# Kernel tuning notes

Measured on AMD Instinct MI355X. Metric: run time of the kernel, lower is better.

Reference implementation:

```python
import jax, jax.numpy as jnp
import numpy as np

N_NODES = 100000
N_EDGES = 1600000
IN_DIM = 128
HEADS = 4
HEAD_DIM = 16  # hidden_dim 64 // 4 heads
HID = HEADS * HEAD_DIM
NEG_SLOPE = 0.2


def setup_inputs() -> dict:
    key = jax.random.key(0)
    ks = jax.random.split(key, 20)
    inp = {
        "x": jax.random.normal(ks[0], (N_NODES, IN_DIM), dtype=jnp.float32),
        "edge_index": jax.random.randint(ks[1], (2, N_EDGES), 0, N_NODES, dtype=jnp.int32),
    }
    dims = [IN_DIM, HID, HID]
    for l in range(3):
        d_in = dims[l]
        sc = 1.0 / np.sqrt(d_in)
        inp[f"w{l}"] = jax.random.normal(ks[2 + 4 * l], (d_in, HID), dtype=jnp.float32) * sc
        inp[f"asrc{l}"] = jax.random.normal(ks[3 + 4 * l], (HEADS, HEAD_DIM), dtype=jnp.float32) * 0.1
        inp[f"adst{l}"] = jax.random.normal(ks[4 + 4 * l], (HEADS, HEAD_DIM), dtype=jnp.float32) * 0.1
        inp[f"b{l}"] = jnp.zeros((HID,), dtype=jnp.float32)
    inp["out_w"] = jax.random.normal(ks[14], (HID, 1), dtype=jnp.float32) * (1.0 / np.sqrt(HID))
    inp["out_b"] = jnp.zeros((1,), dtype=jnp.float32)
    return inp


def _gat_layer(h, src, dst, W, a_src, a_dst, b):
    # h: [N, d_in]; src/dst: [E'] (self-loops already appended)
    n = h.shape[0]
    xh = (h @ W).reshape(n, HEADS, HEAD_DIM)              # [N,H,C]
    al_s = jnp.sum(xh * a_src, axis=-1)                   # [N,H]
    al_d = jnp.sum(xh * a_dst, axis=-1)                   # [N,H]
    e = jax.nn.leaky_relu(al_s[src] + al_d[dst], NEG_SLOPE)  # [E',H]
    # segment-softmax over incoming edges of each destination node
    m = jax.ops.segment_max(e, dst, num_segments=n)       # [N,H]
    p = jnp.exp(e - m[dst])
    z = jax.ops.segment_sum(p, dst, num_segments=n)       # [N,H]
    alpha = p / (z[dst] + 1e-16)                          # [E',H]
    msg = xh[src] * alpha[:, :, None]                     # [E',H,C]
    out = jax.ops.segment_sum(msg, dst, num_segments=n)   # [N,H,C]
    return out.reshape(n, HID) + b


def reference(x, edge_index, w0, asrc0, adst0, b0, w1, asrc1, adst1, b1,
              w2, asrc2, adst2, b2, out_w, out_b):
    n = x.shape[0]
    loops = jnp.arange(n, dtype=edge_index.dtype)
    src = jnp.concatenate([edge_index[0], loops])  # PyG GATConv adds self-loops
    dst = jnp.concatenate([edge_index[1], loops])
    h = x
    params = [(w0, asrc0, adst0, b0), (w1, asrc1, adst1, b1), (w2, asrc2, adst2, b2)]
    for W, a_s, a_d, b in params:
        h = _gat_layer(h, src, dst, W, a_s, a_d, b)
        h = jax.nn.relu(h)
    return (h @ out_w + out_b).squeeze(-1)  # [N]
```

## Files before the change

kernel.cpp:

```cpp
#include <hip/hip_runtime.h>


#define NBMAX 512
#define SCHUNK 4096
#define BCAP 8192

typedef __attribute__((ext_vector_type(8))) short bf16x8;
typedef __attribute__((ext_vector_type(4))) float f32x4;

__device__ inline unsigned short bf16_rtn(float x) {
    union { float f; unsigned u; } a; a.f = x;
    return (unsigned short)((a.u + 0x7FFFu + ((a.u >> 16) & 1u)) >> 16);
}
__device__ inline float bf16_to_f(unsigned short s) {
    union { unsigned u; float f; } b; b.u = ((unsigned)s) << 16;
    return b.f;
}

__global__ __launch_bounds__(256) void k_zero(int* p, int n) {
    int i = blockIdx.x * 256 + threadIdx.x;
    if (i < n) p[i] = 0;
}

__global__ __launch_bounds__(256) void k_bhist(const int* __restrict__ dst, int* __restrict__ bhist, int e) {
    __shared__ unsigned int h[NBMAX];
    int t = threadIdx.x;
    h[t] = 0;
    h[t + 256] = 0;
    __syncthreads();
    for (int i = blockIdx.x * 256 + t; i < e; i += gridDim.x * 256)
        atomicAdd(&h[dst[i] >> 8], 1u);
    __syncthreads();
    if (h[t]) atomicAdd(&bhist[t], (int)h[t]);
    if (h[t + 256]) atomicAdd(&bhist[t + 256], (int)h[t + 256]);
}

__global__ __launch_bounds__(512) void k_bscan(const int* __restrict__ bhist, int* __restrict__ boffs,
                                               int* __restrict__ bfill, int nb, int e) {
    __shared__ int s[NBMAX];
    int t = threadIdx.x;
    int v = (t < nb) ? bhist[t] : 0;
    s[t] = v;
    __syncthreads();
    for (int o = 1; o < 512; o <<= 1) {
        int add = (t >= o) ? s[t - o] : 0;
        __syncthreads();
        s[t] += add;
        __syncthreads();
    }
    boffs[t] = s[t] - v;
    if (t == 511) boffs[512] = s[511];
    bfill[t] = 0;
}

__global__ __launch_bounds__(512) void k_bscatter(const int* __restrict__ src, const int* __restrict__ dst,
                                                  const int* __restrict__ boffs, int* __restrict__ bfill,
                                                  unsigned int* __restrict__ edata, int e) {
    __shared__ unsigned int hist[NBMAX];
    __shared__ unsigned int loc[NBMAX];
    __shared__ int gbase[NBMAX];
    __shared__ unsigned int stmp[NBMAX];
    __shared__ unsigned int sortbuf[SCHUNK];
    __shared__ int posbuf[SCHUNK];
    int t = threadIdx.x;
    int i0 = blockIdx.x * SCHUNK;
    int cnt = min(SCHUNK, e - i0);
    hist[t] = 0;
    __syncthreads();
    for (int j = t; j < cnt; j += 512) atomicAdd(&hist[dst[i0 + j] >> 8], 1u);
    __syncthreads();
    unsigned int v = hist[t];
    stmp[t] = v;
    __syncthreads();
    for (int o = 1; o < 512; o <<= 1) {
        unsigned int add = (t >= o) ? stmp[t - o] : 0;
        __syncthreads();
        stmp[t] += add;
        __syncthreads();
    }
    loc[t] = stmp[t] - v;
    int gb = 0;
    if (v > 0) gb = atomicAdd(&bfill[t], (int)v);
    gbase[t] = boffs[t] + gb - (int)loc[t];
    hist[t] = loc[t];
    __syncthreads();
    for (int j = t; j < cnt; j += 512) {
        int d = dst[i0 + j];
        int s = src[i0 + j];
        int b = d >> 8;
        unsigned int p = atomicAdd(&hist[b], 1u);
        sortbuf[p] = (unsigned int)s | ((unsigned int)(d & 255) << 24);
        posbuf[p] = gbase[b] + (int)p;
    }
    __syncthreads();
    for (int j = t; j < cnt; j += 512) edata[posbuf[j]] = sortbuf[j];
}

__global__ __launch_bounds__(256) void k_bfinal(const unsigned int* __restrict__ edata,
                                                const int* __restrict__ boffs, int* __restrict__ offs,
                                                int* __restrict__ ssrc, int* __restrict__ sdst,
                                                int n, int nb) {
    __shared__ unsigned int hist[256];
    __shared__ unsigned int stmp[256];
    __shared__ unsigned int loc[256];
    __shared__ unsigned int srcbuf[BCAP];
    __shared__ unsigned char dstbuf[BCAP];
    int b = blockIdx.x;
    int t = threadIdx.x;
    int e0 = boffs[b], e1 = boffs[b + 1];
    int cnt = e1 - e0;
    hist[t] = 0;
    __syncthreads();
    for (int j = t; j < cnt; j += 256) atomicAdd(&hist[edata[e0 + j] >> 24], 1u);
    __syncthreads();
    unsigned int v = hist[t];
    stmp[t] = v;
    __syncthreads();
    for (int o = 1; o < 256; o <<= 1) {
        unsigned int add = (t >= o) ? stmp[t - o] : 0;
        __syncthreads();
        stmp[t] += add;
        __syncthreads();
    }
    loc[t] = stmp[t] - v;
    int node = b * 256 + t;
    if (node < n) offs[node] = e0 + (int)loc[t];
    if (b == nb - 1 && t == 0) offs[n] = e1;
    hist[t] = loc[t];
    __syncthreads();
    if (cnt <= BCAP) {
        for (int j = t; j < cnt; j += 256) {
            unsigned int p = edata[e0 + j];
            unsigned int pos = atomicAdd(&hist[p >> 24], 1u);
            srcbuf[pos] = p & 0xFFFFFFu;
            dstbuf[pos] = (unsigned char)(p >> 24);
        }
        __syncthreads();
        for (int j = t; j < cnt; j += 256) {
            ssrc[e0 + j] = (int)srcbuf[j];
            sdst[e0 + j] = b * 256 + (int)dstbuf[j];
        }
    } else {
        for (int j = t; j < cnt; j += 256) {
            unsigned int p = edata[e0 + j];
            unsigned int pos = atomicAdd(&hist[p >> 24], 1u);
            ssrc[e0 + (int)pos] = (int)(p & 0xFFFFFFu);
            sdst[e0 + (int)pos] = b * 256 + (int)(p >> 24);
        }
    }
}

__global__ __launch_bounds__(256) void k_wprep(const float* __restrict__ w0, const float* __restrict__ w1,
                                               const float* __restrict__ w2,
                                               unsigned short* __restrict__ p0h, unsigned short* __restrict__ p0l,
                                               unsigned short* __restrict__ p1h, unsigned short* __restrict__ p1l,
                                               unsigned short* __restrict__ p2h, unsigned short* __restrict__ p2l) {
    int g = blockIdx.x * 256 + threadIdx.x;
    const float* W;
    unsigned short *ph, *pl;
    int idx;
    if (g < 1024) { W = w0; ph = p0h; pl = p0l; idx = g; }
    else if (g < 1536) { W = w1; ph = p1h; pl = p1l; idx = g - 1024; }
    else if (g < 2048) { W = w2; ph = p2h; pl = p2l; idx = g - 1536; }
    else return;
    int ko = idx >> 6, nn = idx & 63;
#pragma unroll
    for (int j = 0; j < 8; ++j) {
        float w = W[(size_t)(ko * 8 + j) * 64 + nn];
        unsigned short hb = bf16_rtn(w);
        ph[(size_t)idx * 8 + j] = hb;
        pl[(size_t)idx * 8 + j] = bf16_rtn(w - bf16_to_f(hb));
    }
}

template <int D_IN>
__global__ __launch_bounds__(256) void k_mgemm(const float* __restrict__ h,
                                               const unsigned short* __restrict__ wph,
                                               const unsigned short* __restrict__ wpl,
                                               const float* __restrict__ asrc, const float* __restrict__ adst,
                                               float* __restrict__ xh, float* __restrict__ als,
                                               float* __restrict__ ald, int n) {
    int t = threadIdx.x;
    int wv = t >> 6, lane = t & 63;
    int quad = lane >> 4, l16 = lane & 15;
    int m0 = blockIdx.x * 64 + wv * 16;
    int node_a = m0 + l16;
    int mm = min(node_a, n - 1);
    const float* hrow = h + (size_t)mm * D_IN + quad * 8;

    f32x4 acc[4];
#pragma unroll
    for (int i = 0; i < 4; ++i) acc[i] = (f32x4){0.f, 0.f, 0.f, 0.f};

    constexpr int KSTEPS = D_IN / 32;
#pragma unroll
    for (int s = 0; s < KSTEPS; ++s) {
        float4 a0 = *(const float4*)(hrow + s * 32);
        float4 a1 = *(const float4*)(hrow + s * 32 + 4);
        float av[8] = {a0.x, a0.y, a0.z, a0.w, a1.x, a1.y, a1.z, a1.w};
        bf16x8 ahi, alo;
#pragma unroll
        for (int j = 0; j < 8; ++j) {
            unsigned short hb = bf16_rtn(av[j]);
            ahi[j] = (short)hb;
            alo[j] = (short)bf16_rtn(av[j] - bf16_to_f(hb));
        }
        const unsigned short* bbase = wph + ((size_t)((s * 4 + quad) * 64 + l16)) * 8;
        const unsigned short* bbasel = wpl + ((size_t)((s * 4 + quad) * 64 + l16)) * 8;
#pragma unroll
        for (int nt = 0; nt < 4; ++nt) {
            bf16x8 bhi = *(const bf16x8*)(bbase + (size_t)nt * 16 * 8);
            bf16x8 blo = *(const bf16x8*)(bbasel + (size_t)nt * 16 * 8);
            acc[nt] = __builtin_amdgcn_mfma_f32_16x16x32_bf16(ahi, bhi, acc[nt], 0, 0, 0);
            acc[nt] = __builtin_amdgcn_mfma_f32_16x16x32_bf16(ahi, blo, acc[nt], 0, 0, 0);
            acc[nt] = __builtin_amdgcn_mfma_f32_16x16x32_bf16(alo, bhi, acc[nt], 0, 0, 0);
        }
    }
#pragma unroll
    for (int nt = 0; nt < 4; ++nt) {
        float as_l = asrc[nt * 16 + l16];
        float ad_l = adst[nt * 16 + l16];
#pragma unroll
        for (int r = 0; r < 4; ++r) {
            int node = m0 + quad * 4 + r;
            float c = acc[nt][r];
            if (node < n) xh[(size_t)node * 64 + nt * 16 + l16] = c;
            float ps = c * as_l, pd = c * ad_l;
            ps += __shfl_xor(ps, 1, 64); pd += __shfl_xor(pd, 1, 64);
            ps += __shfl_xor(ps, 2, 64); pd += __shfl_xor(pd, 2, 64);
            ps += __shfl_xor(ps, 4, 64); pd += __shfl_xor(pd, 4, 64);
            ps += __shfl_xor(ps, 8, 64); pd += __shfl_xor(pd, 8, 64);
            if (l16 == 0 && node < n) {
                als[node * 4 + nt] = ps;
                ald[node * 4 + nt] = pd;
            }
        }
    }
}

__device__ inline float4 lrelu4(float4 v) {
    float4 r;
    r.x = v.x >= 0.f ? v.x : 0.2f * v.x;
    r.y = v.y >= 0.f ? v.y : 0.2f * v.y;
    r.z = v.z >= 0.f ? v.z : 0.2f * v.z;
    r.w = v.w >= 0.f ? v.w : 0.2f * v.w;
    return r;
}

__global__ __launch_bounds__(256) void k_edge(const int* __restrict__ ssrc, const int* __restrict__ sdst,
                                              const float* __restrict__ als, const float* __restrict__ ald,
                                              float* __restrict__ pei, int e) {
    int j = blockIdx.x * 256 + threadIdx.x;
    if (j >= e) return;
    int u = ssrc[j], d = sdst[j];
    float4 alu = *(const float4*)(als + 4 * (size_t)u);
    float4 asd = *(const float4*)(als + 4 * (size_t)d);
    float4 add4 = *(const float4*)(ald + 4 * (size_t)d);
    float4 m4 = lrelu4(make_float4(asd.x + add4.x, asd.y + add4.y, asd.z + add4.z, asd.w + add4.w));
    float4 e4 = lrelu4(make_float4(alu.x + add4.x, alu.y + add4.y, alu.z + add4.z, alu.w + add4.w));
    float4 pe;
    pe.x = __expf(e4.x - m4.x);
    pe.y = __expf(e4.y - m4.y);
    pe.z = __expf(e4.z - m4.z);
    pe.w = __expf(e4.w - m4.w);
    *(float4*)(pei + 4 * (size_t)j) = pe;
}

__global__ __launch_bounds__(256) void k_agg(const float* __restrict__ xh, const float* __restrict__ pei,
                                             const int* __restrict__ offs, const int* __restrict__ ssrc,
                                             const float* __restrict__ bias, float* __restrict__ hout,
                                             const float* __restrict__ outw, const float* __restrict__ outb,
                                             float* __restrict__ fout, int n) {
    __shared__ int s_u[4][64];
    __shared__ float s_pe[4][4][64];
    int wslot = threadIdx.x >> 6;
    int lane = threadIdx.x & 63;
    int v = (blockIdx.x * 256 + threadIdx.x) >> 6;
    if (v >= n) return;
    int head = lane >> 4;
    int* ub = s_u[wslot];
    float* per = s_pe[wslot][head];
    float* pew = &s_pe[wslot][0][lane];

    int start = offs[v], end = offs[v + 1];
    const char* xl = (const char*)(xh + lane);
    float acc = *(const float*)(xl + ((size_t)(unsigned)v << 8));
    float zsum = 0.f;

    for (int s0 = start; s0 < end; s0 += 64) {
        int cnt = min(64, end - s0);
        bool act = lane < cnt;
        int u = v;
        float4 pe = make_float4(0.f, 0.f, 0.f, 0.f);
        if (act) {
            u = ssrc[s0 + lane];
            pe = *(const float4*)(pei + 4 * (size_t)(s0 + lane));
        }
        ub[lane] = u << 8;
        pew[0] = pe.x;
        pew[64] = pe.y;
        pew[128] = pe.z;
        pew[192] = pe.w;
        int ng = (cnt + 3) >> 2;
        int g = 0;
        for (; g + 2 <= ng; g += 2) {
            int4 uu0 = *(const int4*)&ub[g * 4];
            int4 uu1 = *(const int4*)&ub[g * 4 + 4];
            float4 pp0 = *(const float4*)&per[g * 4];
            float4 pp1 = *(const float4*)&per[g * 4 + 4];
            float x0 = *(const float*)(xl + (size_t)(unsigned)uu0.x);
            float x1 = *(const float*)(xl + (size_t)(unsigned)uu0.y);
            float x2 = *(const float*)(xl + (size_t)(unsigned)uu0.z);
            float x3 = *(const float*)(xl + (size_t)(unsigned)uu0.w);
            float x4 = *(const float*)(xl + (size_t)(unsigned)uu1.x);
            float x5 = *(const float*)(xl + (size_t)(unsigned)uu1.y);
            float x6 = *(const float*)(xl + (size_t)(unsigned)uu1.z);
            float x7 = *(const float*)(xl + (size_t)(unsigned)uu1.w);
            zsum += pp0.x + pp0.y + pp0.z + pp0.w;
            zsum += pp1.x + pp1.y + pp1.z + pp1.w;
            acc += pp0.x * x0; acc += pp0.y * x1; acc += pp0.z * x2; acc += pp0.w * x3;
            acc += pp1.x * x4; acc += pp1.y * x5; acc += pp1.z * x6; acc += pp1.w * x7;
        }
        for (; g < ng; ++g) {
            int4 uu = *(const int4*)&ub[g * 4];
            float4 pp = *(const float4*)&per[g * 4];
            float x0 = *(const float*)(xl + (size_t)(unsigned)uu.x);
            float x1 = *(const float*)(xl + (size_t)(unsigned)uu.y);
            float x2 = *(const float*)(xl + (size_t)(unsigned)uu.z);
            float x3 = *(const float*)(xl + (size_t)(unsigned)uu.w);
            zsum += pp.x + pp.y + pp.z + pp.w;
            acc += pp.x * x0; acc += pp.y * x1; acc += pp.z * x2; acc += pp.w * x3;
        }
    }
    float z = 1.f + zsum;
    float o = acc / (z + 1e-16f) + bias[lane];
    o = fmaxf(o, 0.f);
    if (outw) {
        float tsum = o * outw[lane];
#pragma unroll
        for (int d = 32; d; d >>= 1) tsum += __shfl_down(tsum, d, 64);
        if (lane == 0) fout[v] = tsum + outb[0];
    } else {
        hout[((size_t)v << 6) + lane] = o;
    }
}

extern "C" void kernel_launch(void* const* d_in, const int* in_sizes, int n_in,
                              void* d_out, int out_size, void* d_ws, size_t ws_size,
                              hipStream_t stream) {
    const float* x = (const float*)d_in[0];
    const int* ei = (const int*)d_in[1];
    const float* w[3] = {(const float*)d_in[2], (const float*)d_in[6], (const float*)d_in[10]};
    const float* as[3] = {(const float*)d_in[3], (const float*)d_in[7], (const float*)d_in[11]};
    const float* ad[3] = {(const float*)d_in[4], (const float*)d_in[8], (const float*)d_in[12]};
    const float* b[3] = {(const float*)d_in[5], (const float*)d_in[9], (const float*)d_in[13]};
    const float* outw = (const float*)d_in[14];
    const float* outb = (const float*)d_in[15];

    const int N = in_sizes[0] / 128;
    const int E = in_sizes[1] / 2;
    const int* src = ei;
    const int* dst = ei + E;
    const int NB = (N + 255) / 256;

    char* ws = (char*)d_ws;
    auto alloc = [&](size_t bytes) -> void* {
        void* p = (void*)ws;
        ws += (bytes + 255) & ~(size_t)255;
        return p;
    };
    int* bhist = (int*)alloc(NBMAX * 4);
    int* boffs = (int*)alloc((NBMAX + 1) * 4);
    int* bfill = (int*)alloc(NBMAX * 4);
    int* offs = (int*)alloc((size_t)(N + 1) * 4);
    int* ssrc = (int*)alloc((size_t)E * 4);
    int* sdst = (int*)alloc((size_t)E * 4);
    float* pei = (float*)alloc((size_t)E * 4 * 4);
    float* xh = (float*)alloc((size_t)N * 64 * 4);
    float* hbuf = (float*)alloc((size_t)N * 64 * 4);
    float* als = (float*)alloc((size_t)N * 4 * 4);
    float* ald = (float*)alloc((size_t)N * 4 * 4);
    unsigned short* p0h = (unsigned short*)alloc(8192 * 2);
    unsigned short* p0l = (unsigned short*)alloc(8192 * 2);
    unsigned short* p1h = (unsigned short*)alloc(4096 * 2);
    unsigned short* p1l = (unsigned short*)alloc(4096 * 2);
    unsigned short* p2h = (unsigned short*)alloc(4096 * 2);
    unsigned short* p2l = (unsigned short*)alloc(4096 * 2);
    unsigned int* edata = (unsigned int*)xh;

    k_wprep<<<8, 256, 0, stream>>>(w[0], w[1], w[2], p0h, p0l, p1h, p1l, p2h, p2l);
    k_zero<<<(NBMAX + 255) / 256, 256, 0, stream>>>(bhist, NBMAX);
    k_bhist<<<256, 256, 0, stream>>>(dst, bhist, E);
    k_bscan<<<1, 512, 0, stream>>>(bhist, boffs, bfill, NB, E);
    k_bscatter<<<(E + SCHUNK - 1) / SCHUNK, 512, 0, stream>>>(src, dst, boffs, bfill, edata, E);
    k_bfinal<<<NB, 256, 0, stream>>>(edata, boffs, offs, ssrc, sdst, N, NB);

    const int gblocks = (N + 63) / 64;
    const int ablocks = (N + 3) / 4;
    const int eblocks = (E + 255) / 256;

    k_mgemm<128><<<gblocks, 256, 0, stream>>>(x, p0h, p0l, as[0], ad[0], xh, als, ald, N);
    k_edge<<<eblocks, 256, 0, stream>>>(ssrc, sdst, als, ald, pei, E);
    k_agg<<<ablocks, 256, 0, stream>>>(xh, pei, offs, ssrc, b[0], hbuf, nullptr, nullptr, nullptr, N);
    k_mgemm<64><<<gblocks, 256, 0, stream>>>(hbuf, p1h, p1l, as[1], ad[1], xh, als, ald, N);
    k_edge<<<eblocks, 256, 0, stream>>>(ssrc, sdst, als, ald, pei, E);
    k_agg<<<ablocks, 256, 0, stream>>>(xh, pei, offs, ssrc, b[1], hbuf, nullptr, nullptr, nullptr, N);
    k_mgemm<64><<<gblocks, 256, 0, stream>>>(hbuf, p2h, p2l, as[2], ad[2], xh, als, ald, N);
    k_edge<<<eblocks, 256, 0, stream>>>(ssrc, sdst, als, ald, pei, E);
    k_agg<<<ablocks, 256, 0, stream>>>(xh, pei, offs, ssrc, b[2], nullptr, outw, outb, (float*)d_out, N);
}
```

Measured before the change: 447.5 us.

## Fuse edge attention exp computation into aggregation kernel and drop sdst

Removes the separate per-edge kernel that wrote exp scores to a global buffer, and computes the scores inside the aggregation kernel from the per-node attention logits. The softmax shift uses the self-loop logit of the destination node, as before. The sorted destination array is no longer produced, which removes a store stream from the sort. The aggregation inner loop is also unrolled to 16 gathers per iteration to keep more loads in flight. The trade is that the aggregation kernel now does extra gathers of als and exp work per edge, in place of three kernel launches and the global write and read of the score buffer per layer.

After: 442.4 us. Within noise of the previous version (-1.1%).

```diff
diff --git a/kernel.cpp b/kernel.cpp
--- a/kernel.cpp
+++ b/kernel.cpp
@@ -98,13 +98,11 @@
 
 __global__ __launch_bounds__(256) void k_bfinal(const unsigned int* __restrict__ edata,
                                                 const int* __restrict__ boffs, int* __restrict__ offs,
-                                                int* __restrict__ ssrc, int* __restrict__ sdst,
-                                                int n, int nb) {
+                                                int* __restrict__ ssrc, int n, int nb) {
     __shared__ unsigned int hist[256];
     __shared__ unsigned int stmp[256];
     __shared__ unsigned int loc[256];
     __shared__ unsigned int srcbuf[BCAP];
-    __shared__ unsigned char dstbuf[BCAP];
     int b = blockIdx.x;
     int t = threadIdx.x;
     int e0 = boffs[b], e1 = boffs[b + 1];
@@ -133,19 +131,14 @@
             unsigned int p = edata[e0 + j];
             unsigned int pos = atomicAdd(&hist[p >> 24], 1u);
             srcbuf[pos] = p & 0xFFFFFFu;
-            dstbuf[pos] = (unsigned char)(p >> 24);
-        }
-        __syncthreads();
-        for (int j = t; j < cnt; j += 256) {
-            ssrc[e0 + j] = (int)srcbuf[j];
-            sdst[e0 + j] = b * 256 + (int)dstbuf[j];
-        }
+        }
+        __syncthreads();
+        for (int j = t; j < cnt; j += 256) ssrc[e0 + j] = (int)srcbuf[j];
     } else {
         for (int j = t; j < cnt; j += 256) {
             unsigned int p = edata[e0 + j];
             unsigned int pos = atomicAdd(&hist[p >> 24], 1u);
             ssrc[e0 + (int)pos] = (int)(p & 0xFFFFFFu);
-            sdst[e0 + (int)pos] = b * 256 + (int)(p >> 24);
         }
     }
 }
@@ -247,26 +240,8 @@
     return r;
 }
 
-__global__ __launch_bounds__(256) void k_edge(const int* __restrict__ ssrc, const int* __restrict__ sdst,
-                                              const float* __restrict__ als, const float* __restrict__ ald,
-                                              float* __restrict__ pei, int e) {
-    int j = blockIdx.x * 256 + threadIdx.x;
-    if (j >= e) return;
-    int u = ssrc[j], d = sdst[j];
-    float4 alu = *(const float4*)(als + 4 * (size_t)u);
-    float4 asd = *(const float4*)(als + 4 * (size_t)d);
-    float4 add4 = *(const float4*)(ald + 4 * (size_t)d);
-    float4 m4 = lrelu4(make_float4(asd.x + add4.x, asd.y + add4.y, asd.z + add4.z, asd.w + add4.w));
-    float4 e4 = lrelu4(make_float4(alu.x + add4.x, alu.y + add4.y, alu.z + add4.z, alu.w + add4.w));
-    float4 pe;
-    pe.x = __expf(e4.x - m4.x);
-    pe.y = __expf(e4.y - m4.y);
-    pe.z = __expf(e4.z - m4.z);
-    pe.w = __expf(e4.w - m4.w);
-    *(float4*)(pei + 4 * (size_t)j) = pe;
-}
-
-__global__ __launch_bounds__(256) void k_agg(const float* __restrict__ xh, const float* __restrict__ pei,
+__global__ __launch_bounds__(256) void k_agg(const float* __restrict__ xh,
+                                             const float* __restrict__ als, const float* __restrict__ ald,
                                              const int* __restrict__ offs, const int* __restrict__ ssrc,
                                              const float* __restrict__ bias, float* __restrict__ hout,
                                              const float* __restrict__ outw, const float* __restrict__ outb,
@@ -283,18 +258,27 @@
     float* pew = &s_pe[wslot][0][lane];
 
     int start = offs[v], end = offs[v + 1];
+    float4 alsv = *(const float4*)(als + 4 * (size_t)v);
+    float4 aldv = *(const float4*)(ald + 4 * (size_t)v);
+    float4 m4 = lrelu4(make_float4(alsv.x + aldv.x, alsv.y + aldv.y,
+                                   alsv.z + aldv.z, alsv.w + aldv.w));
     const char* xl = (const char*)(xh + lane);
     float acc = *(const float*)(xl + ((size_t)(unsigned)v << 8));
     float zsum = 0.f;
 
     for (int s0 = start; s0 < end; s0 += 64) {
         int cnt = min(64, end - s0);
-        bool act = lane < cnt;
         int u = v;
         float4 pe = make_float4(0.f, 0.f, 0.f, 0.f);
-        if (act) {
+        if (lane < cnt) {
             u = ssrc[s0 + lane];
-            pe = *(const float4*)(pei + 4 * (size_t)(s0 + lane));
+            float4 alu = *(const float4*)(als + 4 * (size_t)u);
+            float4 e4 = lrelu4(make_float4(alu.x + aldv.x, alu.y + aldv.y,
+                                           alu.z + aldv.z, alu.w + aldv.w));
+            pe.x = __expf(e4.x - m4.x);
+            pe.y = __expf(e4.y - m4.y);
+            pe.z = __expf(e4.z - m4.z);
+            pe.w = __expf(e4.w - m4.w);
         }
         ub[lane] = u << 8;
         pew[0] = pe.x;
@@ -303,6 +287,40 @@
         pew[192] = pe.w;
         int ng = (cnt + 3) >> 2;
         int g = 0;
+        for (; g + 4 <= ng; g += 4) {
+            int4 uu0 = *(const int4*)&ub[g * 4];
+            int4 uu1 = *(const int4*)&ub[g * 4 + 4];
+            int4 uu2 = *(const int4*)&ub[g * 4 + 8];
+            int4 uu3 = *(const int4*)&ub[g * 4 + 12];
+            float4 pp0 = *(const float4*)&per[g * 4];
+            float4 pp1 = *(const float4*)&per[g * 4 + 4];
+            float4 pp2 = *(const float4*)&per[g * 4 + 8];
+            float4 pp3 = *(const float4*)&per[g * 4 + 12];
+            float x0 = *(const float*)(xl + (size_t)(unsigned)uu0.x);
+            float x1 = *(const float*)(xl + (size_t)(unsigned)uu0.y);
+            float x2 = *(const float*)(xl + (size_t)(unsigned)uu0.z);
+            float x3 = *(const float*)(xl + (size_t)(unsigned)uu0.w);
+            float x4 = *(const float*)(xl + (size_t)(unsigned)uu1.x);
+            float x5 = *(const float*)(xl + (size_t)(unsigned)uu1.y);
+            float x6 = *(const float*)(xl + (size_t)(unsigned)uu1.z);
+            float x7 = *(const float*)(xl + (size_t)(unsigned)uu1.w);
+            float x8 = *(const float*)(xl + (size_t)(unsigned)uu2.x);
+            float x9 = *(const float*)(xl + (size_t)(unsigned)uu2.y);
+            float xa = *(const float*)(xl + (size_t)(unsigned)uu2.z);
+            float xb = *(const float*)(xl + (size_t)(unsigned)uu2.w);
+            float xc = *(const float*)(xl + (size_t)(unsigned)uu3.x);
+            float xd = *(const float*)(xl + (size_t)(unsigned)uu3.y);
+            float xe = *(const float*)(xl + (size_t)(unsigned)uu3.z);
+            float xf = *(const float*)(xl + (size_t)(unsigned)uu3.w);
+            zsum += pp0.x + pp0.y + pp0.z + pp0.w;
+            zsum += pp1.x + pp1.y + pp1.z + pp1.w;
+            zsum += pp2.x + pp2.y + pp2.z + pp2.w;
+            zsum += pp3.x + pp3.y + pp3.z + pp3.w;
+            acc += pp0.x * x0; acc += pp0.y * x1; acc += pp0.z * x2; acc += pp0.w * x3;
+            acc += pp1.x * x4; acc += pp1.y * x5; acc += pp1.z * x6; acc += pp1.w * x7;
+            acc += pp2.x * x8; acc += pp2.y * x9; acc += pp2.z * xa; acc += pp2.w * xb;
+            acc += pp3.x * xc; acc += pp3.y * xd; acc += pp3.z * xe; acc += pp3.w * xf;
+        }
         for (; g + 2 <= ng; g += 2) {
             int4 uu0 = *(const int4*)&ub[g * 4];
             int4 uu1 = *(const int4*)&ub[g * 4 + 4];
@@ -374,8 +392,6 @@
     int* bfill = (int*)alloc(NBMAX * 4);
     int* offs = (int*)alloc((size_t)(N + 1) * 4);
     int* ssrc = (int*)alloc((size_t)E * 4);
-    int* sdst = (int*)alloc((size_t)E * 4);
-    float* pei = (float*)alloc((size_t)E * 4 * 4);
     float* xh = (float*)alloc((size_t)N * 64 * 4);
     float* hbuf = (float*)alloc((size_t)N * 64 * 4);
     float* als = (float*)alloc((size_t)N * 4 * 4);
@@ -393,19 +409,15 @@
     k_bhist<<<256, 256, 0, stream>>>(dst, bhist, E);
     k_bscan<<<1, 512, 0, stream>>>(bhist, boffs, bfill, NB, E);
     k_bscatter<<<(E + SCHUNK - 1) / SCHUNK, 512, 0, stream>>>(src, dst, boffs, bfill, edata, E);
-    k_bfinal<<<NB, 256, 0, stream>>>(edata, boffs, offs, ssrc, sdst, N, NB);
+    k_bfinal<<<NB, 256, 0, stream>>>(edata, boffs, offs, ssrc, N, NB);
 
     const int gblocks = (N + 63) / 64;
     const int ablocks = (N + 3) / 4;
-    const int eblocks = (E + 255) / 256;
 
     k_mgemm<128><<<gblocks, 256, 0, stream>>>(x, p0h, p0l, as[0], ad[0], xh, als, ald, N);
-    k_edge<<<eblocks, 256, 0, stream>>>(ssrc, sdst, als, ald, pei, E);
-    k_agg<<<ablocks, 256, 0, stream>>>(xh, pei, offs, ssrc, b[0], hbuf, nullptr, nullptr, nullptr, N);
+    k_agg<<<ablocks, 256, 0, stream>>>(xh, als, ald, offs, ssrc, b[0], hbuf, nullptr, nullptr, nullptr, N);
     k_mgemm<64><<<gblocks, 256, 0, stream>>>(hbuf, p1h, p1l, as[1], ad[1], xh, als, ald, N);
-    k_edge<<<eblocks, 256, 0, stream>>>(ssrc, sdst, als, ald, pei, E);
-    k_agg<<<ablocks, 256, 0, stream>>>(xh, pei, offs, ssrc, b[1], hbuf, nullptr, nullptr, nullptr, N);
+    k_agg<<<ablocks, 256, 0, stream>>>(xh, als, ald, offs, ssrc, b[1], hbuf, nullptr, nullptr, nullptr, N);
     k_mgemm<64><<<gblocks, 256, 0, stream>>>(hbuf, p2h, p2l, as[2], ad[2], xh, als, ald, N);
-    k_edge<<<eblocks, 256, 0, stream>>>(ssrc, sdst, als, ald, pei, E);
-    k_agg<<<ablocks, 256, 0, stream>>>(xh, pei, offs, ssrc, b[2], nullptr, outw, outb, (float*)d_out, N);
-}
+    k_agg<<<ablocks, 256, 0, stream>>>(xh, als, ald, offs, ssrc, b[2], nullptr, outw, outb, (float*)d_out, N);
+}
```

## Fuse edge softmax scores into aggregation with padded CSR and four nodes per wave

Applied to the files above, without the earlier changes.

Removes the separate per-edge score kernel and its E×4 float intermediate. Aggregation now recomputes the leaky-relu and exp scores from the node attention logits on the fly. Each node's edge segment is padded to a multiple of four, using a sentinel node with a -1e30 score and zero features, so grouped loads need no masking. The sdst array is dropped, and each wavefront now processes four destination nodes and splits the chunk's edges by node boundaries. This trades extra gathers of als/ald and more complex control flow for fewer launches and less global memory traffic.

New measurement: 434.3 us. 3.0% less time.

```diff
diff --git a/kernel.cpp b/kernel.cpp
--- a/kernel.cpp
+++ b/kernel.cpp
@@ -4,6 +4,7 @@
 #define NBMAX 512
 #define SCHUNK 4096
 #define BCAP 8192
+#define PADSLACK 768
 
 typedef __attribute__((ext_vector_type(8))) short bf16x8;
 typedef __attribute__((ext_vector_type(4))) float f32x4;
@@ -17,9 +18,14 @@
     return b.f;
 }
 
-__global__ __launch_bounds__(256) void k_zero(int* p, int n) {
+__global__ __launch_bounds__(256) void k_init(int* __restrict__ bhist, int nb,
+                                              float* __restrict__ als, float* __restrict__ xh, int n) {
     int i = blockIdx.x * 256 + threadIdx.x;
-    if (i < n) p[i] = 0;
+    if (i < nb) bhist[i] = 0;
+    int j = i - NBMAX;
+    if (j >= 0 && j < 4) als[(size_t)n * 4 + j] = -1e30f;
+    int k = i - NBMAX - 4;
+    if (k >= 0 && k < 64) xh[(size_t)n * 64 + k] = 0.f;
 }
 
 __global__ __launch_bounds__(256) void k_bhist(const int* __restrict__ dst, int* __restrict__ bhist, int e) {
@@ -97,24 +103,27 @@
 }
 
 __global__ __launch_bounds__(256) void k_bfinal(const unsigned int* __restrict__ edata,
-                                                const int* __restrict__ boffs, int* __restrict__ offs,
-                                                int* __restrict__ ssrc, int* __restrict__ sdst,
+                                                const int* __restrict__ boffs, int* __restrict__ poffs,
+                                                int* __restrict__ pend, int* __restrict__ ssrc,
                                                 int n, int nb) {
     __shared__ unsigned int hist[256];
     __shared__ unsigned int stmp[256];
     __shared__ unsigned int loc[256];
+    __shared__ unsigned int cnt_s[256];
     __shared__ unsigned int srcbuf[BCAP];
-    __shared__ unsigned char dstbuf[BCAP];
     int b = blockIdx.x;
     int t = threadIdx.x;
     int e0 = boffs[b], e1 = boffs[b + 1];
     int cnt = e1 - e0;
+    int pb = e0 + b * PADSLACK;
     hist[t] = 0;
     __syncthreads();
     for (int j = t; j < cnt; j += 256) atomicAdd(&hist[edata[e0 + j] >> 24], 1u);
     __syncthreads();
     unsigned int v = hist[t];
-    stmp[t] = v;
+    unsigned int v4 = (v + 3u) & ~3u;
+    cnt_s[t] = v;
+    stmp[t] = v4;
     __syncthreads();
     for (int o = 1; o < 256; o <<= 1) {
         unsigned int add = (t >= o) ? stmp[t - o] : 0;
@@ -122,31 +131,31 @@
         stmp[t] += add;
         __syncthreads();
     }
-    loc[t] = stmp[t] - v;
+    loc[t] = stmp[t] - v4;
+    int ptot = (int)stmp[255];
     int node = b * 256 + t;
-    if (node < n) offs[node] = e0 + (int)loc[t];
-    if (b == nb - 1 && t == 0) offs[n] = e1;
+    if (node < n) {
+        poffs[node] = pb + (int)loc[t];
+        pend[node] = pb + (int)(loc[t] + v4);
+    }
     hist[t] = loc[t];
     __syncthreads();
-    if (cnt <= BCAP) {
+    if (cnt + PADSLACK <= BCAP) {
         for (int j = t; j < cnt; j += 256) {
             unsigned int p = edata[e0 + j];
             unsigned int pos = atomicAdd(&hist[p >> 24], 1u);
             srcbuf[pos] = p & 0xFFFFFFu;
-            dstbuf[pos] = (unsigned char)(p >> 24);
-        }
-        __syncthreads();
-        for (int j = t; j < cnt; j += 256) {
-            ssrc[e0 + j] = (int)srcbuf[j];
-            sdst[e0 + j] = b * 256 + (int)dstbuf[j];
-        }
+        }
+        for (unsigned int k = v; k < v4; ++k) srcbuf[loc[t] + k] = (unsigned int)n;
+        __syncthreads();
+        for (int j = t; j < ptot; j += 256) ssrc[pb + j] = (int)srcbuf[j];
     } else {
         for (int j = t; j < cnt; j += 256) {
             unsigned int p = edata[e0 + j];
             unsigned int pos = atomicAdd(&hist[p >> 24], 1u);
-            ssrc[e0 + (int)pos] = (int)(p & 0xFFFFFFu);
-            sdst[e0 + (int)pos] = b * 256 + (int)(p >> 24);
-        }
+            ssrc[pb + (int)pos] = (int)(p & 0xFFFFFFu);
+        }
+        for (unsigned int k = v; k < v4; ++k) ssrc[pb + (int)(loc[t] + k)] = n;
     }
 }
 
@@ -247,27 +256,59 @@
     return r;
 }
 
-__global__ __launch_bounds__(256) void k_edge(const int* __restrict__ ssrc, const int* __restrict__ sdst,
-                                              const float* __restrict__ als, const float* __restrict__ ald,
-                                              float* __restrict__ pei, int e) {
-    int j = blockIdx.x * 256 + threadIdx.x;
-    if (j >= e) return;
-    int u = ssrc[j], d = sdst[j];
-    float4 alu = *(const float4*)(als + 4 * (size_t)u);
-    float4 asd = *(const float4*)(als + 4 * (size_t)d);
-    float4 add4 = *(const float4*)(ald + 4 * (size_t)d);
-    float4 m4 = lrelu4(make_float4(asd.x + add4.x, asd.y + add4.y, asd.z + add4.z, asd.w + add4.w));
-    float4 e4 = lrelu4(make_float4(alu.x + add4.x, alu.y + add4.y, alu.z + add4.z, alu.w + add4.w));
-    float4 pe;
-    pe.x = __expf(e4.x - m4.x);
-    pe.y = __expf(e4.y - m4.y);
-    pe.z = __expf(e4.z - m4.z);
-    pe.w = __expf(e4.w - m4.w);
-    *(float4*)(pei + 4 * (size_t)j) = pe;
-}
-
-__global__ __launch_bounds__(256) void k_agg(const float* __restrict__ xh, const float* __restrict__ pei,
-                                             const int* __restrict__ offs, const int* __restrict__ ssrc,
+#define ACCUM(LO, HI, ACC, ZS)                                                  \
+    {                                                                           \
+        int g_ = ((LO) - s0) >> 2, gb_ = ((HI) - s0) >> 2;                      \
+        for (; g_ + 4 <= gb_; g_ += 4) {                                        \
+            int4 uu0 = *(const int4*)&ub[g_ * 4];                               \
+            int4 uu1 = *(const int4*)&ub[g_ * 4 + 4];                           \
+            int4 uu2 = *(const int4*)&ub[g_ * 4 + 8];                           \
+            int4 uu3 = *(const int4*)&ub[g_ * 4 + 12];                          \
+            float4 pp0 = *(const float4*)&per[g_ * 4];                          \
+            float4 pp1 = *(const float4*)&per[g_ * 4 + 4];                      \
+            float4 pp2 = *(const float4*)&per[g_ * 4 + 8];                      \
+            float4 pp3 = *(const float4*)&per[g_ * 4 + 12];                     \
+            float x0 = *(const float*)(xl + (size_t)(unsigned)uu0.x);           \
+            float x1 = *(const float*)(xl + (size_t)(unsigned)uu0.y);           \
+            float x2 = *(const float*)(xl + (size_t)(unsigned)uu0.z);           \
+            float x3 = *(const float*)(xl + (size_t)(unsigned)uu0.w);           \
+            float x4 = *(const float*)(xl + (size_t)(unsigned)uu1.x);           \
+            float x5 = *(const float*)(xl + (size_t)(unsigned)uu1.y);           \
+            float x6 = *(const float*)(xl + (size_t)(unsigned)uu1.z);           \
+            float x7 = *(const float*)(xl + (size_t)(unsigned)uu1.w);           \
+            float x8 = *(const float*)(xl + (size_t)(unsigned)uu2.x);           \
+            float x9 = *(const float*)(xl + (size_t)(unsigned)uu2.y);           \
+            float xa = *(const float*)(xl + (size_t)(unsigned)uu2.z);           \
+            float xb = *(const float*)(xl + (size_t)(unsigned)uu2.w);           \
+            float xc = *(const float*)(xl + (size_t)(unsigned)uu3.x);           \
+            float xd = *(const float*)(xl + (size_t)(unsigned)uu3.y);           \
+            float xe = *(const float*)(xl + (size_t)(unsigned)uu3.z);           \
+            float xf = *(const float*)(xl + (size_t)(unsigned)uu3.w);           \
+            ZS += pp0.x + pp0.y + pp0.z + pp0.w;                                \
+            ZS += pp1.x + pp1.y + pp1.z + pp1.w;                                \
+            ZS += pp2.x + pp2.y + pp2.z + pp2.w;                                \
+            ZS += pp3.x + pp3.y + pp3.z + pp3.w;                                \
+            ACC += pp0.x * x0; ACC += pp0.y * x1; ACC += pp0.z * x2; ACC += pp0.w * x3; \
+            ACC += pp1.x * x4; ACC += pp1.y * x5; ACC += pp1.z * x6; ACC += pp1.w * x7; \
+            ACC += pp2.x * x8; ACC += pp2.y * x9; ACC += pp2.z * xa; ACC += pp2.w * xb; \
+            ACC += pp3.x * xc; ACC += pp3.y * xd; ACC += pp3.z * xe; ACC += pp3.w * xf; \
+        }                                                                       \
+        for (; g_ < gb_; ++g_) {                                                \
+            int4 uu = *(const int4*)&ub[g_ * 4];                                \
+            float4 pp = *(const float4*)&per[g_ * 4];                           \
+            float x0 = *(const float*)(xl + (size_t)(unsigned)uu.x);            \
+            float x1 = *(const float*)(xl + (size_t)(unsigned)uu.y);            \
+            float x2 = *(const float*)(xl + (size_t)(unsigned)uu.z);            \
+            float x3 = *(const float*)(xl + (size_t)(unsigned)uu.w);            \
+            ZS += pp.x + pp.y + pp.z + pp.w;                                    \
+            ACC += pp.x * x0; ACC += pp.y * x1; ACC += pp.z * x2; ACC += pp.w * x3; \
+        }                                                                       \
+    }
+
+__global__ __launch_bounds__(256) void k_agg(const float* __restrict__ xh,
+                                             const float* __restrict__ als, const float* __restrict__ ald,
+                                             const int* __restrict__ poffs, const int* __restrict__ pend,
+                                             const int* __restrict__ ssrc,
                                              const float* __restrict__ bias, float* __restrict__ hout,
                                              const float* __restrict__ outw, const float* __restrict__ outb,
                                              float* __restrict__ fout, int n) {
@@ -275,73 +316,93 @@
     __shared__ float s_pe[4][4][64];
     int wslot = threadIdx.x >> 6;
     int lane = threadIdx.x & 63;
-    int v = (blockIdx.x * 256 + threadIdx.x) >> 6;
-    if (v >= n) return;
+    int w = (blockIdx.x * 256 + threadIdx.x) >> 6;
+    int v0 = w << 2;
+    if (v0 >= n) return;
     int head = lane >> 4;
     int* ub = s_u[wslot];
     float* per = s_pe[wslot][head];
     float* pew = &s_pe[wslot][0][lane];
 
-    int start = offs[v], end = offs[v + 1];
+    int vlast = n - 1;
+    int last = min(v0 + 3, vlast);
+    int4 rr = *(const int4*)(poffs + v0);
+    int e3 = pend[last];
+    int r0 = rr.x;
+    int r1 = (v0 + 1 <= last) ? rr.y : e3;
+    int r2 = (v0 + 2 <= last) ? rr.z : e3;
+    int r3 = (v0 + 3 <= last) ? rr.w : e3;
+
     const char* xl = (const char*)(xh + lane);
-    float acc = *(const float*)(xl + ((size_t)(unsigned)v << 8));
-    float zsum = 0.f;
-
-    for (int s0 = start; s0 < end; s0 += 64) {
-        int cnt = min(64, end - s0);
-        bool act = lane < cnt;
-        int u = v;
-        float4 pe = make_float4(0.f, 0.f, 0.f, 0.f);
-        if (act) {
-            u = ssrc[s0 + lane];
-            pe = *(const float4*)(pei + 4 * (size_t)(s0 + lane));
-        }
+    float acc0 = *(const float*)(xl + ((size_t)(unsigned)v0 << 8));
+    float acc1 = *(const float*)(xl + ((size_t)(unsigned)min(v0 + 1, vlast) << 8));
+    float acc2 = *(const float*)(xl + ((size_t)(unsigned)min(v0 + 2, vlast) << 8));
+    float acc3 = *(const float*)(xl + ((size_t)(unsigned)min(v0 + 3, vlast) << 8));
+    float zs0 = 0.f, zs1 = 0.f, zs2 = 0.f, zs3 = 0.f;
+
+    for (int s0 = r0; s0 < e3; s0 += 64) {
+        int cnt = min(64, e3 - s0);
+        int e = s0 + lane;
+        int u = n;
+        if (lane < cnt) u = ssrc[e];
+        int nid = v0 + (e >= r1) + (e >= r2) + (e >= r3);
+        nid = min(nid, vlast);
+        float4 alsd = *(const float4*)(als + 4 * (size_t)nid);
+        float4 aldd = *(const float4*)(ald + 4 * (size_t)nid);
+        float4 m4 = lrelu4(make_float4(alsd.x + aldd.x, alsd.y + aldd.y,
+                                       alsd.z + aldd.z, alsd.w + aldd.w));
+        float4 alu = *(const float4*)(als + 4 * (size_t)u);
+        float4 e4 = lrelu4(make_float4(alu.x + aldd.x, alu.y + aldd.y,
+                                       alu.z + aldd.z, alu.w + aldd.w));
+        float4 pe;
+        pe.x = __expf(e4.x - m4.x);
+        pe.y = __expf(e4.y - m4.y);
+        pe.z = __expf(e4.z - m4.z);
+        pe.w = __expf(e4.w - m4.w);
         ub[lane] = u << 8;
         pew[0] = pe.x;
         pew[64] = pe.y;
         pew[128] = pe.z;
         pew[192] = pe.w;
-        int ng = (cnt + 3) >> 2;
-        int g = 0;
-        for (; g + 2 <= ng; g += 2) {
-            int4 uu0 = *(const int4*)&ub[g * 4];
-            int4 uu1 = *(const int4*)&ub[g * 4 + 4];
-            float4 pp0 = *(const float4*)&per[g * 4];
-            float4 pp1 = *(const float4*)&per[g * 4 + 4];
-            float x0 = *(const float*)(xl + (size_t)(unsigned)uu0.x);
-            float x1 = *(const float*)(xl + (size_t)(unsigned)uu0.y);
-            float x2 = *(const float*)(xl + (size_t)(unsigned)uu0.z);
-            float x3 = *(const float*)(xl + (size_t)(unsigned)uu0.w);
-            float x4 = *(const float*)(xl + (size_t)(unsigned)uu1.x);
-            float x5 = *(const float*)(xl + (size_t)(unsigned)uu1.y);
-            float x6 = *(const float*)(xl + (size_t)(unsigned)uu1.z);
-            float x7 = *(const float*)(xl + (size_t)(unsigned)uu1.w);
-            zsum += pp0.x + pp0.y + pp0.z + pp0.w;
-            zsum += pp1.x + pp1.y + pp1.z + pp1.w;
-            acc += pp0.x * x0; acc += pp0.y * x1; acc += pp0.z * x2; acc += pp0.w * x3;
-            acc += pp1.x * x4; acc += pp1.y * x5; acc += pp1.z * x6; acc += pp1.w * x7;
-        }
-        for (; g < ng; ++g) {
-            int4 uu = *(const int4*)&ub[g * 4];
-            float4 pp = *(const float4*)&per[g * 4];
-            float x0 = *(const float*)(xl + (size_t)(unsigned)uu.x);
-            float x1 = *(const float*)(xl + (size_t)(unsigned)uu.y);
-            float x2 = *(const float*)(xl + (size_t)(unsigned)uu.z);
-            float x3 = *(const float*)(xl + (size_t)(unsigned)uu.w);
-            zsum += pp.x + pp.y + pp.z + pp.w;
-            acc += pp.x * x0; acc += pp.y * x1; acc += pp.z * x2; acc += pp.w * x3;
-        }
-    }
-    float z = 1.f + zsum;
-    float o = acc / (z + 1e-16f) + bias[lane];
-    o = fmaxf(o, 0.f);
+        int lim = s0 + cnt;
+        int hi0 = min(r1, lim);
+        int lo1 = max(r1, s0), hi1 = min(r2, lim);
+        int lo2 = max(r2, s0), hi2 = min(r3, lim);
+        int lo3 = max(r3, s0);
+        ACCUM(s0, hi0, acc0, zs0);
+        ACCUM(lo1, hi1, acc1, zs1);
+        ACCUM(lo2, hi2, acc2, zs2);
+        ACCUM(lo3, lim, acc3, zs3);
+    }
+
+    float bl = bias[lane];
+    float z0 = 1.f + zs0, z1 = 1.f + zs1, z2 = 1.f + zs2, z3 = 1.f + zs3;
+    float o0 = fmaxf(acc0 / (z0 + 1e-16f) + bl, 0.f);
+    float o1 = fmaxf(acc1 / (z1 + 1e-16f) + bl, 0.f);
+    float o2 = fmaxf(acc2 / (z2 + 1e-16f) + bl, 0.f);
+    float o3 = fmaxf(acc3 / (z3 + 1e-16f) + bl, 0.f);
     if (outw) {
-        float tsum = o * outw[lane];
-#pragma unroll
-        for (int d = 32; d; d >>= 1) tsum += __shfl_down(tsum, d, 64);
-        if (lane == 0) fout[v] = tsum + outb[0];
+        float ow = outw[lane];
+        float ob = outb[0];
+        float t0 = o0 * ow, t1 = o1 * ow, t2 = o2 * ow, t3 = o3 * ow;
+#pragma unroll
+        for (int d = 32; d; d >>= 1) {
+            t0 += __shfl_down(t0, d, 64);
+            t1 += __shfl_down(t1, d, 64);
+            t2 += __shfl_down(t2, d, 64);
+            t3 += __shfl_down(t3, d, 64);
+        }
+        if (lane == 0) {
+            fout[v0] = t0 + ob;
+            if (v0 + 1 < n) fout[v0 + 1] = t1 + ob;
+            if (v0 + 2 < n) fout[v0 + 2] = t2 + ob;
+            if (v0 + 3 < n) fout[v0 + 3] = t3 + ob;
+        }
     } else {
-        hout[((size_t)v << 6) + lane] = o;
+        hout[((size_t)v0 << 6) + lane] = o0;
+        if (v0 + 1 < n) hout[((size_t)(v0 + 1) << 6) + lane] = o1;
+        if (v0 + 2 < n) hout[((size_t)(v0 + 2) << 6) + lane] = o2;
+        if (v0 + 3 < n) hout[((size_t)(v0 + 3) << 6) + lane] = o3;
     }
 }
 
@@ -372,13 +433,12 @@
     int* bhist = (int*)alloc(NBMAX * 4);
     int* boffs = (int*)alloc((NBMAX + 1) * 4);
     int* bfill = (int*)alloc(NBMAX * 4);
-    int* offs = (int*)alloc((size_t)(N + 1) * 4);
-    int* ssrc = (int*)alloc((size_t)E * 4);
-    int* sdst = (int*)alloc((size_t)E * 4);
-    float* pei = (float*)alloc((size_t)E * 4 * 4);
-    float* xh = (float*)alloc((size_t)N * 64 * 4);
+    int* poffs = (int*)alloc((size_t)(N + 8) * 4);
+    int* pend = (int*)alloc((size_t)N * 4);
+    int* ssrc = (int*)alloc((size_t)(E + NBMAX * PADSLACK + 256) * 4);
+    float* xh = (float*)alloc((size_t)(N + 1) * 64 * 4);
     float* hbuf = (float*)alloc((size_t)N * 64 * 4);
-    float* als = (float*)alloc((size_t)N * 4 * 4);
+    float* als = (float*)alloc((size_t)(N + 1) * 4 * 4);
     float* ald = (float*)alloc((size_t)N * 4 * 4);
     unsigned short* p0h = (unsigned short*)alloc(8192 * 2);
     unsigned short* p0l = (unsigned short*)alloc(8192 * 2);
@@ -389,23 +449,19 @@
     unsigned int* edata = (unsigned int*)xh;
 
     k_wprep<<<8, 256, 0, stream>>>(w[0], w[1], w[2], p0h, p0l, p1h, p1l, p2h, p2l);
-    k_zero<<<(NBMAX + 255) / 256, 256, 0, stream>>>(bhist, NBMAX);
+    k_init<<<3, 256, 0, stream>>>(bhist, NBMAX, als, xh, N);
     k_bhist<<<256, 256, 0, stream>>>(dst, bhist, E);
     k_bscan<<<1, 512, 0, stream>>>(bhist, boffs, bfill, NB, E);
     k_bscatter<<<(E + SCHUNK - 1) / SCHUNK, 512, 0, stream>>>(src, dst, boffs, bfill, edata, E);
-    k_bfinal<<<NB, 256, 0, stream>>>(edata, boffs, offs, ssrc, sdst, N, NB);
+    k_bfinal<<<NB, 256, 0, stream>>>(edata, boffs, poffs, pend, ssrc, N, NB);
 
     const int gblocks = (N + 63) / 64;
-    const int ablocks = (N + 3) / 4;
-    const int eblocks = (E + 255) / 256;
+    const int ablocks = (N + 15) / 16;
 
     k_mgemm<128><<<gblocks, 256, 0, stream>>>(x, p0h, p0l, as[0], ad[0], xh, als, ald, N);
-    k_edge<<<eblocks, 256, 0, stream>>>(ssrc, sdst, als, ald, pei, E);
-    k_agg<<<ablocks, 256, 0, stream>>>(xh, pei, offs, ssrc, b[0], hbuf, nullptr, nullptr, nullptr, N);
+    k_agg<<<ablocks, 256, 0, stream>>>(xh, als, ald, poffs, pend, ssrc, b[0], hbuf, nullptr, nullptr, nullptr, N);
     k_mgemm<64><<<gblocks, 256, 0, stream>>>(hbuf, p1h, p1l, as[1], ad[1], xh, als, ald, N);
-    k_edge<<<eblocks, 256, 0, stream>>>(ssrc, sdst, als, ald, pei, E);
-    k_agg<<<ablocks, 256, 0, stream>>>(xh, pei, offs, ssrc, b[1], hbuf, nullptr, nullptr, nullptr, N);
+    k_agg<<<ablocks, 256, 0, stream>>>(xh, als, ald, poffs, pend, ssrc, b[1], hbuf, nullptr, nullptr, nullptr, N);
     k_mgemm<64><<<gblocks, 256, 0, stream>>>(hbuf, p2h, p2l, as[2], ad[2], xh, als, ald, N);
-    k_edge<<<eblocks, 256, 0, stream>>>(ssrc, sdst, als, ald, pei, E);
-    k_agg<<<ablocks, 256, 0, stream>>>(xh, pei, offs, ssrc, b[2], nullptr, outw, outb, (float*)d_out, N);
-}
+    k_agg<<<ablocks, 256, 0, stream>>>(xh, als, ald, poffs, pend, ssrc, b[2], nullptr, outw, outb, (float*)d_out, N);
+}
```
